# Optimization experiments

Measured on AMD Instinct MI355X. Metric: run time of the kernel, lower is better.

The kernel has to match this reference:

```python
import jax, jax.numpy as jnp
import numpy as np

B, S, D = 4, 2048, 1024
H, DK, DV = 16, 64, 64


def setup_inputs() -> dict:
    key = jax.random.key(0)
    ks = jax.random.split(key, 9)
    std = 1.0 / np.sqrt(D)
    inp = {
        "x": jax.random.normal(ks[0], (B, S, D), jnp.float32),
        "c": jax.random.normal(ks[1], (B, S, D), jnp.float32),
        "Wq_x": jax.random.normal(ks[2], (D, H * DK), jnp.float32) * std,
        "Wk_x": jax.random.normal(ks[3], (D, H * DK), jnp.float32) * std,
        "Wv_x": jax.random.normal(ks[4], (D, H * DV), jnp.float32) * std,
        "Wq_c": jax.random.normal(ks[5], (D, H * DK), jnp.float32) * std,
        "Wk_c": jax.random.normal(ks[6], (D, H * DK), jnp.float32) * std,
        "Wv_c": jax.random.normal(ks[7], (D, H * DV), jnp.float32) * std,
        "W_proj": jax.random.normal(ks[8], (2 * H * DV, D), jnp.float32) * (1.0 / np.sqrt(2 * H * DV)),
        "b_proj": jnp.zeros((D,), jnp.float32),
    }
    return inp


def _heads(t, hd):
    # [B,S,H*hd] -> [B,H,S,hd]
    b, s, _ = t.shape
    return t.reshape(b, s, H, hd).transpose(0, 2, 1, 3)


def reference(x, c, Wq_x, Wk_x, Wv_x, Wq_c, Wk_c, Wv_c, W_proj, b_proj):
    q = jnp.concatenate([_heads(x @ Wq_x, DK), _heads(c @ Wq_c, DK)], axis=-1)  # [B,H,S,2DK]
    k = jnp.concatenate([_heads(x @ Wk_x, DK), _heads(c @ Wk_c, DK)], axis=-1)
    v = jnp.concatenate([_heads(x @ Wv_x, DV), _heads(c @ Wv_c, DV)], axis=-1)  # [B,H,S,2DV]
    # NOTE: original scales by sqrt(k_dim), not sqrt(2*k_dim) (faithful)
    scores = jnp.einsum("bhqd,bhkd->bhqk", q, k) / np.float32(np.sqrt(DK))
    attn = jax.nn.softmax(scores, axis=-1)
    out = jnp.einsum("bhqk,bhkd->bhqd", attn, v)  # [B,H,S,2DV]
    out = out.transpose(0, 2, 1, 3).reshape(x.shape[0], x.shape[1], -1)  # [B,S,H*2DV]
    return out @ W_proj + b_proj
```

## Files before the change

### kernel.cpp

```cpp
#include <hip/hip_runtime.h>
#include <hip/hip_bf16.h>
#include <stdint.h>

#define BB 4
#define SS 2048
#define DD 1024
#define HH 16
#define DHH 128

typedef __bf16 bf16x8 __attribute__((ext_vector_type(8)));
typedef __bf16 bf16x4 __attribute__((ext_vector_type(4)));
typedef float  f32x4  __attribute__((ext_vector_type(4)));

#define SL2E 0.180336880111186f

#if __has_builtin(__builtin_amdgcn_exp2f)
#define EXP2(x) __builtin_amdgcn_exp2f(x)
#else
#define EXP2(x) exp2f(x)
#endif

#define GLOAD_LDS16(gp, lp) \
  __builtin_amdgcn_global_load_lds((const __attribute__((address_space(1))) unsigned int*)(gp), \
                                   (__attribute__((address_space(3))) unsigned int*)(lp), 16, 0, 0)

__global__ void cast2_kernel(const float* __restrict__ x, const float* __restrict__ c,
                             __bf16* __restrict__ out, int n) {
    int i = (blockIdx.x * blockDim.x + threadIdx.x) * 4;
    const float* src = (i < n) ? (x + i) : (c + (i - n));
    f32x4 v = *(const f32x4*)src;
    bf16x4 o;
    o[0] = (__bf16)v[0]; o[1] = (__bf16)v[1]; o[2] = (__bf16)v[2]; o[3] = (__bf16)v[3];
    *(bf16x4*)(out + i) = o;
}

__global__ void transpose_cast_kernel(const float* __restrict__ in, __bf16* __restrict__ out,
                                      int K, int N) {
    __shared__ float tile[32][33];
    int n0 = blockIdx.x * 32, k0 = blockIdx.y * 32;
    int tx = threadIdx.x, ty = threadIdx.y;
    #pragma unroll
    for (int i = 0; i < 32; i += 8)
        tile[ty + i][tx] = in[(size_t)(k0 + ty + i) * N + n0 + tx];
    __syncthreads();
    #pragma unroll
    for (int i = 0; i < 32; i += 8)
        out[(size_t)(n0 + ty + i) * K + k0 + tx] = (__bf16)tile[tx][ty + i];
}

__global__ void transpose6_kernel(const float* s0, const float* s1, const float* s2,
                                  const float* s3, const float* s4, const float* s5,
                                  __bf16* __restrict__ dst) {
    const float* srcs[6] = {s0, s1, s2, s3, s4, s5};
    const float* __restrict__ in = srcs[blockIdx.z];
    __bf16* __restrict__ out = dst + (size_t)blockIdx.z * 1024 * 1024;
    __shared__ float tile[32][33];
    int n0 = blockIdx.x * 32, k0 = blockIdx.y * 32;
    int tx = threadIdx.x, ty = threadIdx.y;
    #pragma unroll
    for (int i = 0; i < 32; i += 8)
        tile[ty + i][tx] = in[(size_t)(k0 + ty + i) * 1024 + n0 + tx];
    __syncthreads();
    #pragma unroll
    for (int i = 0; i < 32; i += 8)
        out[(size_t)(n0 + ty + i) * 1024 + k0 + tx] = (__bf16)tile[tx][ty + i];
}

template <int EPI>
__global__ void gemm128_kernel(const __bf16* __restrict__ A0, const __bf16* __restrict__ A1,
                               const __bf16* __restrict__ B0, const __bf16* __restrict__ B1,
                               int K, void* __restrict__ outp,
                               const float* __restrict__ bias) {
    const int z = blockIdx.z;
    const __bf16* __restrict__ A  = z ? A1 : A0;
    const __bf16* __restrict__ Bt = z ? B1 : B0;
    const int qkv_off = z * 64;

    __shared__ __bf16 As[128][32];
    __shared__ __bf16 Bs[128][32];
    const int t = threadIdx.x;
    const int wave = t >> 6, lane = t & 63;
    const int l15 = lane & 15, quad = lane >> 4;
    const int wm = (wave & 1) * 64, wn = (wave >> 1) * 64;
    const int m0 = blockIdx.x * 128, n0 = blockIdx.y * 128;
    const int lrow = lane >> 2;
    const int lcol = (lane & 3) * 8;

    f32x4 acc[4][4] = {};

    for (int k0 = 0; k0 < K; k0 += 32) {
        #pragma unroll
        for (int c2 = 0; c2 < 2; ++c2) {
            int rb = (wave * 2 + c2) * 16;
            GLOAD_LDS16(A  + (size_t)(m0 + rb + lrow) * K + k0 + lcol, &As[rb][0]);
            GLOAD_LDS16(Bt + (size_t)(n0 + rb + lrow) * K + k0 + lcol, &Bs[rb][0]);
        }
        __syncthreads();
        bf16x8 af[4], bfv[4];
        #pragma unroll
        for (int i = 0; i < 4; ++i) af[i]  = *(const bf16x8*)&As[wm + i * 16 + l15][quad * 8];
        #pragma unroll
        for (int i = 0; i < 4; ++i) bfv[i] = *(const bf16x8*)&Bs[wn + i * 16 + l15][quad * 8];
        #pragma unroll
        for (int mi = 0; mi < 4; ++mi)
            #pragma unroll
            for (int ni = 0; ni < 4; ++ni)
                acc[mi][ni] = __builtin_amdgcn_mfma_f32_16x16x32_bf16(af[mi], bfv[ni], acc[mi][ni], 0, 0, 0);
        __syncthreads();
    }

    const size_t nQKV = (size_t)BB * HH * SS * DHH;
    #pragma unroll
    for (int mi = 0; mi < 4; ++mi) {
        #pragma unroll
        for (int ni = 0; ni < 4; ++ni) {
            #pragma unroll
            for (int rr = 0; rr < 4; ++rr) {
                int m = m0 + wm + mi * 16 + quad * 4 + rr;
                int n = n0 + wn + ni * 16 + l15;
                if (EPI == 1) {
                    float* o = (float*)outp;
                    o[(size_t)m * 1024 + n] = acc[mi][ni][rr] + bias[n];
                } else if (EPI == 2) {
                    int h = m >> 6, dl = m & 63;
                    int b = n >> 11, s = n & (SS - 1);
                    __bf16* vt = (__bf16*)outp;
                    vt[(((size_t)b * HH + h) * DHH + dl + qkv_off) * SS + s] = (__bf16)acc[mi][ni][rr];
                } else {
                    int b = m >> 11, s = m & (SS - 1);
                    int n1 = n & 1023;
                    int h = n1 >> 6, d = (n1 & 63) + qkv_off;
                    if (n < 1024) {
                        __bf16* q = (__bf16*)outp;
                        q[(((size_t)b * HH + h) * SS + s) * DHH + d] = (__bf16)(acc[mi][ni][rr] * SL2E);
                    } else {
                        int dsw = (((d >> 3) ^ (s & 15)) << 3) | (d & 7);
                        __bf16* kq = (__bf16*)outp + nQKV;
                        kq[(((size_t)b * HH + h) * SS + s) * DHH + dsw] = (__bf16)acc[mi][ni][rr];
                    }
                }
            }
        }
    }
}

#define LDS_VT 16384
__global__ __launch_bounds__(256, 3)
void attn_kernel(const __bf16* __restrict__ Q, const __bf16* __restrict__ Kg,
                 const __bf16* __restrict__ Vg, __bf16* __restrict__ O) {
    __shared__ __align__(16) char smem[32768];

    const int t = threadIdx.x;
    const int wave = t >> 6, lane = t & 63;
    const int l15 = lane & 15, quad = lane >> 4;
    const int bh = blockIdx.y;
    const int b = bh >> 4, h = bh & 15;
    const int mt = blockIdx.x;
    const size_t base  = (size_t)bh * SS * DHH;
    const size_t vbase = (size_t)bh * DHH * SS;

    int kaddr[4];
    #pragma unroll
    for (int kst = 0; kst < 4; ++kst)
        kaddr[kst] = l15 * 256 + (((4 * kst + quad) ^ l15) & 15) * 16;
    int vaddr[2];
    #pragma unroll
    for (int hf = 0; hf < 2; ++hf)
        vaddr[hf] = LDS_VT + l15 * 128 + (((4 * hf + quad) ^ (l15 & 7)) & 7) * 16;
    int pw[2];
    #pragma unroll
    for (int nl = 0; nl < 2; ++nl)
        pw[nl] = (wave * 32 + quad * 4) * 64 +
                 (((2 * nl + (l15 >> 3)) ^ quad) & 3) * 16 + (l15 & 7) * 2;
    const int par = (wave * 32 + l15) * 64 + ((quad ^ (l15 >> 2)) & 3) * 16;

    const __bf16* kstage = Kg + base + (size_t)wave * 2048 + lane * 8;
    const __bf16* vstage = Vg + vbase + (size_t)(wave * 32 + (lane >> 3)) * SS
                           + ((lane & 7) ^ ((lane >> 3) & 7)) * 8;

    bf16x8 qf[2][4];
    #pragma unroll
    for (int ms = 0; ms < 2; ++ms) {
        int row = mt * 128 + wave * 32 + ms * 16 + l15;
        #pragma unroll
        for (int kst = 0; kst < 4; ++kst)
            qf[ms][kst] = *(const bf16x8*)(Q + base + (size_t)row * DHH + kst * 32 + quad * 8);
    }

    f32x4 oacc[2][8] = {};
    float li_[2][4] = {};

    for (int kt = 0; kt < SS / 64; ++kt) {
        #pragma unroll
        for (int i = 0; i < 4; ++i)
            GLOAD_LDS16(kstage + (size_t)kt * 8192 + i * 512,
                        smem + wave * 4096 + i * 1024);
        #pragma unroll
        for (int i = 0; i < 4; ++i)
            GLOAD_LDS16(vstage + kt * 64 + (size_t)i * 8 * SS,
                        smem + LDS_VT + wave * 4096 + i * 1024);
        __syncthreads();

        #pragma unroll
        for (int hf = 0; hf < 2; ++hf) {
            f32x4 sx[2][2] = {};
            #pragma unroll
            for (int kst = 0; kst < 4; ++kst) {
                bf16x8 kf0 = *(const bf16x8*)(smem + kaddr[kst] + 8192 * hf);
                bf16x8 kf1 = *(const bf16x8*)(smem + kaddr[kst] + 8192 * hf + 4096);
                sx[0][0] = __builtin_amdgcn_mfma_f32_16x16x32_bf16(qf[0][kst], kf0, sx[0][0], 0, 0, 0);
                sx[1][0] = __builtin_amdgcn_mfma_f32_16x16x32_bf16(qf[1][kst], kf0, sx[1][0], 0, 0, 0);
                sx[0][1] = __builtin_amdgcn_mfma_f32_16x16x32_bf16(qf[0][kst], kf1, sx[0][1], 0, 0, 0);
                sx[1][1] = __builtin_amdgcn_mfma_f32_16x16x32_bf16(qf[1][kst], kf1, sx[1][1], 0, 0, 0);
            }
            #pragma unroll
            for (int ms = 0; ms < 2; ++ms)
                #pragma unroll
                for (int nl = 0; nl < 2; ++nl)
                    #pragma unroll
                    for (int rr = 0; rr < 4; ++rr) {
                        float p = EXP2(sx[ms][nl][rr]);
                        li_[ms][rr] += p;
                        sx[ms][nl][rr] = p;
                    }
            __syncthreads();

            #pragma unroll
            for (int ms = 0; ms < 2; ++ms)
                #pragma unroll
                for (int nl = 0; nl < 2; ++nl)
                    #pragma unroll
                    for (int rr = 0; rr < 4; ++rr)
                        *(__bf16*)(smem + pw[nl] + 8192 * hf + 1024 * ms + 64 * rr)
                            = (__bf16)sx[ms][nl][rr];

            bf16x8 pa0 = *(const bf16x8*)(smem + par + 8192 * hf);
            bf16x8 pa1 = *(const bf16x8*)(smem + par + 8192 * hf + 1024);
            #pragma unroll
            for (int ds = 0; ds < 8; ++ds) {
                bf16x8 vf = *(const bf16x8*)(smem + vaddr[hf] + 2048 * ds);
                oacc[0][ds] = __builtin_amdgcn_mfma_f32_16x16x32_bf16(pa0, vf, oacc[0][ds], 0, 0, 0);
                oacc[1][ds] = __builtin_amdgcn_mfma_f32_16x16x32_bf16(pa1, vf, oacc[1][ds], 0, 0, 0);
            }
        }
        __syncthreads();
    }

    #pragma unroll
    for (int ms = 0; ms < 2; ++ms)
        #pragma unroll
        for (int rr = 0; rr < 4; ++rr) {
            float v = li_[ms][rr];
            v += __shfl_xor(v, 1);
            v += __shfl_xor(v, 2);
            v += __shfl_xor(v, 4);
            v += __shfl_xor(v, 8);
            li_[ms][rr] = 1.f / v;
        }

    #pragma unroll
    for (int ms = 0; ms < 2; ++ms)
        #pragma unroll
        for (int rr = 0; rr < 4; ++rr) {
            int s = mt * 128 + wave * 32 + ms * 16 + quad * 4 + rr;
            size_t ob = ((size_t)b * SS + s) * (HH * DHH) + (size_t)h * DHH;
            #pragma unroll
            for (int ds = 0; ds < 8; ++ds)
                O[ob + ds * 16 + l15] = (__bf16)(oacc[ms][ds][rr] * li_[ms][rr]);
        }
}

extern "C" void kernel_launch(void* const* d_in, const int* in_sizes, int n_in,
                              void* d_out, int out_size, void* d_ws, size_t ws_size,
                              hipStream_t stream) {
    const float* x      = (const float*)d_in[0];
    const float* c      = (const float*)d_in[1];
    const float* Wq_x   = (const float*)d_in[2];
    const float* Wk_x   = (const float*)d_in[3];
    const float* Wv_x   = (const float*)d_in[4];
    const float* Wq_c   = (const float*)d_in[5];
    const float* Wk_c   = (const float*)d_in[6];
    const float* Wv_c   = (const float*)d_in[7];
    const float* W_proj = (const float*)d_in[8];
    const float* b_proj = (const float*)d_in[9];

    const size_t nXC  = (size_t)BB * SS * DD;
    const size_t nW   = (size_t)DD * DD;
    const size_t nWP  = (size_t)(2 * HH * 64) * DD;
    const size_t nQKV = (size_t)BB * HH * SS * DHH;

    __bf16* ws  = (__bf16*)d_ws;
    __bf16* xb  = ws;
    __bf16* cb  = xb + nXC;
    __bf16* wt0 = cb + nXC;
    __bf16* wt2 = wt0 + 2 * nW;
    __bf16* wt3 = wt0 + 3 * nW;
    __bf16* wt5 = wt0 + 5 * nW;
    __bf16* wtp = wt0 + 6 * nW;
    __bf16* Qb  = wtp + nWP;
    __bf16* Kb  = Qb + nQKV;
    __bf16* Vb  = Kb + nQKV;
    __bf16* Ob  = xb;

    cast2_kernel<<<(int)(2 * nXC / 1024), 256, 0, stream>>>(x, c, xb, (int)nXC);

    transpose6_kernel<<<dim3(32, 32, 6), dim3(32, 8), 0, stream>>>(
        Wq_x, Wk_x, Wv_x, Wq_c, Wk_c, Wv_c, wt0);
    transpose_cast_kernel<<<dim3(32, 64), dim3(32, 8), 0, stream>>>(W_proj, wtp, 2048, 1024);

    gemm128_kernel<4><<<dim3(64, 16, 2), 256, 0, stream>>>(xb, cb, wt0, wt3, 1024, Qb, nullptr);
    gemm128_kernel<2><<<dim3(8, 64, 2), 256, 0, stream>>>(wt2, wt5, xb, cb, 1024, Vb, nullptr);

    attn_kernel<<<dim3(16, 64), 256, 0, stream>>>(Qb, Kb, Vb, Ob);

    gemm128_kernel<1><<<dim3(64, 8, 1), 256, 0, stream>>>(Ob, nullptr, wtp, nullptr, 2048, d_out, b_proj);
}
```

Before: 492.0 us.

## Double-buffer K/V tiles in LDS with separate P scratch and MFMA priority hints

The attention loop now prefetches the next K/V tile into a second LDS buffer while the current tile is being computed, so there is one barrier per tile instead of a load-then-wait pattern. The P tile moves to its own LDS region so it no longer overwrites K, which removes the mid-tile barrier. s_setprio is raised around the MFMA sections to favour matrix issue. LDS use grows to 72KB and occupancy is cut from 3 to 2 blocks per CU. P is written and read per wave within its own rows, so relying on wave-local ordering without a barrier may be safe.

```diff
diff --git a/kernel.cpp b/kernel.cpp
--- a/kernel.cpp
+++ b/kernel.cpp
@@ -144,11 +144,13 @@
     }
 }
 
-#define LDS_VT 16384
-__global__ __launch_bounds__(256, 3)
+#define LDS_BUFSZ 32768
+#define LDS_VT    16384
+#define LDS_PS    65536
+__global__ __launch_bounds__(256, 2)
 void attn_kernel(const __bf16* __restrict__ Q, const __bf16* __restrict__ Kg,
                  const __bf16* __restrict__ Vg, __bf16* __restrict__ O) {
-    __shared__ __align__(16) char smem[32768];
+    __shared__ __align__(16) char smem[73728];
 
     const int t = threadIdx.x;
     const int wave = t >> 6, lane = t & 63;
@@ -170,14 +172,25 @@
     int pw[2];
     #pragma unroll
     for (int nl = 0; nl < 2; ++nl)
-        pw[nl] = (wave * 32 + quad * 4) * 64 +
+        pw[nl] = LDS_PS + (wave * 32 + quad * 4) * 64 +
                  (((2 * nl + (l15 >> 3)) ^ quad) & 3) * 16 + (l15 & 7) * 2;
-    const int par = (wave * 32 + l15) * 64 + ((quad ^ (l15 >> 2)) & 3) * 16;
+    const int par = LDS_PS + (wave * 32 + l15) * 64 + ((quad ^ (l15 >> 2)) & 3) * 16;
 
     const __bf16* kstage = Kg + base + (size_t)wave * 2048 + lane * 8;
     const __bf16* vstage = Vg + vbase + (size_t)(wave * 32 + (lane >> 3)) * SS
                            + ((lane & 7) ^ ((lane >> 3) & 7)) * 8;
 
+    #define STAGE_KV(kt_, bo_) do { \
+        _Pragma("unroll") \
+        for (int i_ = 0; i_ < 4; ++i_) \
+            GLOAD_LDS16(kstage + (size_t)(kt_) * 8192 + i_ * 512, \
+                        smem + (bo_) + wave * 4096 + i_ * 1024); \
+        _Pragma("unroll") \
+        for (int i_ = 0; i_ < 4; ++i_) \
+            GLOAD_LDS16(vstage + (kt_) * 64 + (size_t)i_ * 8 * SS, \
+                        smem + (bo_) + LDS_VT + wave * 4096 + i_ * 1024); \
+    } while (0)
+
     bf16x8 qf[2][4];
     #pragma unroll
     for (int ms = 0; ms < 2; ++ms) {
@@ -190,29 +203,27 @@
     f32x4 oacc[2][8] = {};
     float li_[2][4] = {};
 
+    STAGE_KV(0, 0);
+    __syncthreads();
+
     for (int kt = 0; kt < SS / 64; ++kt) {
-        #pragma unroll
-        for (int i = 0; i < 4; ++i)
-            GLOAD_LDS16(kstage + (size_t)kt * 8192 + i * 512,
-                        smem + wave * 4096 + i * 1024);
-        #pragma unroll
-        for (int i = 0; i < 4; ++i)
-            GLOAD_LDS16(vstage + kt * 64 + (size_t)i * 8 * SS,
-                        smem + LDS_VT + wave * 4096 + i * 1024);
-        __syncthreads();
+        const int co = (kt & 1) * LDS_BUFSZ;
+        if (kt + 1 < SS / 64) STAGE_KV(kt + 1, co ^ LDS_BUFSZ);
 
         #pragma unroll
         for (int hf = 0; hf < 2; ++hf) {
             f32x4 sx[2][2] = {};
+            __builtin_amdgcn_s_setprio(1);
             #pragma unroll
             for (int kst = 0; kst < 4; ++kst) {
-                bf16x8 kf0 = *(const bf16x8*)(smem + kaddr[kst] + 8192 * hf);
-                bf16x8 kf1 = *(const bf16x8*)(smem + kaddr[kst] + 8192 * hf + 4096);
+                bf16x8 kf0 = *(const bf16x8*)(smem + co + kaddr[kst] + 8192 * hf);
+                bf16x8 kf1 = *(const bf16x8*)(smem + co + kaddr[kst] + 8192 * hf + 4096);
                 sx[0][0] = __builtin_amdgcn_mfma_f32_16x16x32_bf16(qf[0][kst], kf0, sx[0][0], 0, 0, 0);
                 sx[1][0] = __builtin_amdgcn_mfma_f32_16x16x32_bf16(qf[1][kst], kf0, sx[1][0], 0, 0, 0);
                 sx[0][1] = __builtin_amdgcn_mfma_f32_16x16x32_bf16(qf[0][kst], kf1, sx[0][1], 0, 0, 0);
                 sx[1][1] = __builtin_amdgcn_mfma_f32_16x16x32_bf16(qf[1][kst], kf1, sx[1][1], 0, 0, 0);
             }
+            __builtin_amdgcn_s_setprio(0);
             #pragma unroll
             for (int ms = 0; ms < 2; ++ms)
                 #pragma unroll
@@ -223,7 +234,6 @@
                         li_[ms][rr] += p;
                         sx[ms][nl][rr] = p;
                     }
-            __syncthreads();
 
             #pragma unroll
             for (int ms = 0; ms < 2; ++ms)
@@ -231,20 +241,23 @@
                 for (int nl = 0; nl < 2; ++nl)
                     #pragma unroll
                     for (int rr = 0; rr < 4; ++rr)
-                        *(__bf16*)(smem + pw[nl] + 8192 * hf + 1024 * ms + 64 * rr)
+                        *(__bf16*)(smem + pw[nl] + 1024 * ms + 64 * rr)
                             = (__bf16)sx[ms][nl][rr];
 
-            bf16x8 pa0 = *(const bf16x8*)(smem + par + 8192 * hf);
-            bf16x8 pa1 = *(const bf16x8*)(smem + par + 8192 * hf + 1024);
+            bf16x8 pa0 = *(const bf16x8*)(smem + par);
+            bf16x8 pa1 = *(const bf16x8*)(smem + par + 1024);
+            __builtin_amdgcn_s_setprio(1);
             #pragma unroll
             for (int ds = 0; ds < 8; ++ds) {
-                bf16x8 vf = *(const bf16x8*)(smem + vaddr[hf] + 2048 * ds);
+                bf16x8 vf = *(const bf16x8*)(smem + co + vaddr[hf] + 2048 * ds);
                 oacc[0][ds] = __builtin_amdgcn_mfma_f32_16x16x32_bf16(pa0, vf, oacc[0][ds], 0, 0, 0);
                 oacc[1][ds] = __builtin_amdgcn_mfma_f32_16x16x32_bf16(pa1, vf, oacc[1][ds], 0, 0, 0);
             }
+            __builtin_amdgcn_s_setprio(0);
         }
         __syncthreads();
     }
+    #undef STAGE_KV
 
     #pragma unroll
     for (int ms = 0; ms < 2; ++ms)
```

After: 475.4 us. 1.04x faster.
